# Optimization experiments

Measured on AMD Instinct MI355X. Metric: run time of the kernel, lower is better.

Reference implementation:

```python
import jax, jax.numpy as jnp
import numpy as np

B, N, F, H, L = 64, 8192, 64, 64, 2  # batch, max_nodes, feature_dim, hidden_dim, n_layers


def setup_inputs() -> dict:
    key = jax.random.key(0)
    k0, k1, k2 = jax.random.split(key, 3)
    s = 0.05
    return {
        "tree_features": jax.random.normal(k0, (B, N, F), dtype=jnp.float32),
        "W_emb": (jax.random.normal(k1, (H, F), dtype=jnp.float32) * s),
        "b_emb": jnp.zeros((H,), dtype=jnp.float32),
        # Wx[l, g] for g in (input, output, cell) gates; forget gate is dead when no children
        "Wx": (jax.random.normal(k2, (L, 3, H, H), dtype=jnp.float32) * s),
        "bW": jnp.zeros((L, 3, H), dtype=jnp.float32),
        # U(h_sum) with h_sum == 0 reduces to the U bias; U weights get zero grad, omitted
        "bU": jnp.zeros((L, 3, H), dtype=jnp.float32),
    }


def reference(tree_features, W_emb, b_emb, Wx, bW, bU):
    # node embedding: [B, N, F] @ [F, H]^T -> [B, N, H]
    h = jnp.einsum('bnf,hf->bnh', tree_features, W_emb) + b_emb
    n_layers = Wx.shape[0]
    for l in range(n_layers):
        # children_h is empty -> h_sum = 0, so U_*(h_sum) = bU (bias only)
        z = jnp.einsum('bni,goi->bngo', h, Wx[l]) + bW[l] + bU[l]  # [B, N, 3, H]
        i = jax.nn.sigmoid(z[:, :, 0])
        o = jax.nn.sigmoid(z[:, :, 1])
        c_tilde = jnp.tanh(z[:, :, 2])
        c = i * c_tilde  # no forget-gate terms: children_c is empty
        h = o * jnp.tanh(c)
    return jnp.mean(h, axis=1)  # [B, H]
```

## Files before the change

### kernel.cpp

```cpp
#include <hip/hip_runtime.h>
#include <hip/hip_bf16.h>


typedef __attribute__((ext_vector_type(4))) float f32x4;
typedef __attribute__((ext_vector_type(8))) short s16x8;
typedef __attribute__((ext_vector_type(4))) short s16x4;

#if __has_builtin(__builtin_amdgcn_rcpf)
#define RCPF(x) __builtin_amdgcn_rcpf(x)
#else
#define RCPF(x) (1.0f / (x))
#endif

__device__ __forceinline__ unsigned short f2h(float f) {
    _Float16 h = (_Float16)f;
    return __builtin_bit_cast(unsigned short, h);
}

__device__ __forceinline__ float gate_h(float z0, float z1, float z2) {
    float s0 = z0 * z0, s1 = z1 * z1, s2 = z2 * z2;
    float n0 = z0 * (s0 + 60.f), d0 = fmaf(24.f, s0, 240.f);
    float n1 = z1 * (s1 + 60.f), d1 = fmaf(24.f, s1, 240.f);
    float n2 = z2 * (s2 + 15.f), d2 = fmaf(6.f, s2, 15.f);
    float P = fmaf(0.5f, d0, n0) * n2;
    float c = P * RCPF(d0 * d2);
    float sc = c * c;
    float nt = c * (sc + 15.f), dt = fmaf(6.f, sc, 15.f);
    float R = fmaf(0.5f, d1, n1) * nt;
    return R * RCPF(d1 * dt);
}

__global__ void prep_weights(const float* __restrict__ W_emb,
                             const float* __restrict__ b_emb,
                             const float* __restrict__ Wx,
                             const float* __restrict__ bW,
                             const float* __restrict__ bU,
                             unsigned short* __restrict__ wfrag,
                             float* __restrict__ wbias) {
    int t = blockIdx.x * 256 + threadIdx.x;
    if (t < 448) {
        int mat = t >> 6, o = t & 63;
        wbias[t] = (mat == 0) ? b_emb[o] : (bW[(mat - 1) * 64 + o] + bU[(mat - 1) * 64 + o]);
    }
    if (t < 28672) {
        int j = t & 7, lane = (t >> 3) & 63, fid = t >> 9;
        int kk = fid & 1, wv = (fid >> 1) & 3, mat = fid >> 3;
        int o = wv * 16 + (lane & 15);
        int k = ((lane >> 4) << 3) + kk * 32 + j;
        float v = (mat == 0) ? W_emb[o * 64 + k] : Wx[(mat - 1) * 4096 + o * 64 + k];
        wfrag[t] = f2h(v);
    }
}

__global__ __launch_bounds__(256, 2) void tree_encoder_mfma(
        const float* __restrict__ tree,
        const unsigned short* __restrict__ wfrag,
        const float* __restrict__ wbias,
        float* __restrict__ out) {
    __shared__ unsigned short x16[4096];
    __shared__ unsigned short hA[4096], hB[4096];
    __shared__ float biasL[448];
    const int tid = threadIdx.x;
    const int w = tid >> 6, lane = tid & 63;
    const int lg = lane >> 4, lr = lane & 15;

    for (int i = tid; i < 448; i += 256) biasL[i] = wbias[i];

    s16x8 wA[14];
#pragma unroll
    for (int m = 0; m < 7; ++m)
#pragma unroll
        for (int kk = 0; kk < 2; ++kk)
            wA[m * 2 + kk] = *(const s16x8*)(wfrag + (((m * 4 + w) * 2 + kk) << 9) + lane * 8);
#pragma unroll
    for (int m = 0; m < 14; ++m) asm volatile("" : "+v"(wA[m]));

    int ro[4][2], wo[4];
#pragma unroll
    for (int nt = 0; nt < 4; ++nt) {
        const int n = nt * 16 + lr, sw = (n & 7) << 3;
        ro[nt][0] = (n << 6) + ((lg << 3) ^ sw);
        ro[nt][1] = (n << 6) + (((lg + 4) << 3) ^ sw);
        wo[nt] = (n << 6) + ((w * 16 + 4 * lg) ^ sw);
    }
    const int nc = tid >> 2;
    const int qc = tid & 3;
    const int co0 = (nc << 6) + (((2 * qc) ^ (nc & 7)) << 3);
    const int co1 = (nc << 6) + (((2 * qc + 1) ^ (nc & 7)) << 3);

    float nsum[4] = {0.f, 0.f, 0.f, 0.f};
    const int t0 = blockIdx.x * 4;

    f32x4 xp[4];
    {
        const float* src = tree + ((size_t)t0 << 12) + (tid << 4);
#pragma unroll
        for (int v = 0; v < 4; ++v) xp[v] = *(const f32x4*)(src + 4 * v);
    }

#pragma unroll 1
    for (int ti = 0; ti < 4; ++ti) {
        {
            s16x8 v0, v1;
#pragma unroll
            for (int j = 0; j < 8; ++j) {
                v0[j] = (short)f2h(xp[j >> 2][j & 3]);
                v1[j] = (short)f2h(xp[2 + (j >> 2)][j & 3]);
            }
            *(s16x8*)&x16[co0] = v0;
            *(s16x8*)&x16[co1] = v1;
        }
        if (ti < 3) {
            const float* src = tree + ((size_t)(t0 + ti + 1) << 12) + (tid << 4);
#pragma unroll
            for (int v = 0; v < 4; ++v) xp[v] = *(const f32x4*)(src + 4 * v);
        }
        __syncthreads();

        {
            const f32x4 be = *(const f32x4*)&biasL[w * 16 + 4 * lg];
            f32x4 acc[4];
#pragma unroll
            for (int nt = 0; nt < 4; ++nt) acc[nt] = be;
#pragma unroll
            for (int nt = 0; nt < 4; ++nt)
#pragma unroll
                for (int kk = 0; kk < 2; ++kk) {
                    s16x8 b = *(const s16x8*)&x16[ro[nt][kk]];
                    acc[nt] = __builtin_amdgcn_mfma_f32_16x16x32_f16(wA[kk], b, acc[nt], 0, 0, 0);
                }
#pragma unroll
            for (int nt = 0; nt < 4; ++nt) {
                s16x4 p;
#pragma unroll
                for (int r = 0; r < 4; ++r) p[r] = (short)f2h(acc[nt][r]);
                *(s16x4*)&hA[wo[nt]] = p;
            }
        }
        __syncthreads();

        {
            const f32x4 b0 = *(const f32x4*)&biasL[64 + w * 16 + 4 * lg];
            const f32x4 b1 = *(const f32x4*)&biasL[128 + w * 16 + 4 * lg];
            const f32x4 b2 = *(const f32x4*)&biasL[192 + w * 16 + 4 * lg];
#pragma unroll
            for (int nt = 0; nt < 4; ++nt) {
                f32x4 a0 = b0, a1 = b1, a2 = b2;
#pragma unroll
                for (int kk = 0; kk < 2; ++kk) {
                    s16x8 b = *(const s16x8*)&hA[ro[nt][kk]];
                    a0 = __builtin_amdgcn_mfma_f32_16x16x32_f16(wA[2 + kk], b, a0, 0, 0, 0);
                    a1 = __builtin_amdgcn_mfma_f32_16x16x32_f16(wA[4 + kk], b, a1, 0, 0, 0);
                    a2 = __builtin_amdgcn_mfma_f32_16x16x32_f16(wA[6 + kk], b, a2, 0, 0, 0);
                }
                s16x4 p;
#pragma unroll
                for (int r = 0; r < 4; ++r)
                    p[r] = (short)f2h(gate_h(a0[r], a1[r], a2[r]));
                *(s16x4*)&hB[wo[nt]] = p;
            }
        }
        __syncthreads();

        {
            const f32x4 b0 = *(const f32x4*)&biasL[256 + w * 16 + 4 * lg];
            const f32x4 b1 = *(const f32x4*)&biasL[320 + w * 16 + 4 * lg];
            const f32x4 b2 = *(const f32x4*)&biasL[384 + w * 16 + 4 * lg];
#pragma unroll
            for (int nt = 0; nt < 4; ++nt) {
                f32x4 a0 = b0, a1 = b1, a2 = b2;
#pragma unroll
                for (int kk = 0; kk < 2; ++kk) {
                    s16x8 b = *(const s16x8*)&hB[ro[nt][kk]];
                    a0 = __builtin_amdgcn_mfma_f32_16x16x32_f16(wA[8 + kk], b, a0, 0, 0, 0);
                    a1 = __builtin_amdgcn_mfma_f32_16x16x32_f16(wA[10 + kk], b, a1, 0, 0, 0);
                    a2 = __builtin_amdgcn_mfma_f32_16x16x32_f16(wA[12 + kk], b, a2, 0, 0, 0);
                }
#pragma unroll
                for (int r = 0; r < 4; ++r)
                    nsum[r] += gate_h(a0[r], a1[r], a2[r]);
            }
        }
    }

#pragma unroll
    for (int r = 0; r < 4; ++r) {
        float s = nsum[r];
        s += __shfl_xor(s, 1);
        s += __shfl_xor(s, 2);
        s += __shfl_xor(s, 4);
        s += __shfl_xor(s, 8);
        if (lr == 0)
            atomicAdd(&out[(blockIdx.x >> 5) * 64 + w * 16 + 4 * lg + r], s * (1.0f / 8192.0f));
    }
}

extern "C" void kernel_launch(void* const* d_in, const int* in_sizes, int n_in,
                              void* d_out, int out_size, void* d_ws, size_t ws_size,
                              hipStream_t stream) {
    const float* tree  = (const float*)d_in[0];
    const float* W_emb = (const float*)d_in[1];
    const float* b_emb = (const float*)d_in[2];
    const float* Wx    = (const float*)d_in[3];
    const float* bW    = (const float*)d_in[4];
    const float* bU    = (const float*)d_in[5];
    float* outp = (float*)d_out;
    unsigned short* wfrag = (unsigned short*)d_ws;
    float* wbias = (float*)((char*)d_ws + 57344);

    hipMemsetAsync(d_out, 0, (size_t)out_size * sizeof(float), stream);
    prep_weights<<<112, 256, 0, stream>>>(W_emb, b_emb, Wx, bW, bU, wfrag, wbias);
    tree_encoder_mfma<<<2048, 256, 0, stream>>>(tree, wfrag, wbias, outp);
}
```

Before: 70.53 us.

## Halve grid with 8 tiles per block, raise occupancy, use packed fp16 converts

Each block now processes 8 tiles of 64 nodes instead of 4, so the grid shrinks to 1024 blocks and the atomic output index changes to match. The register prefetch of the next tile is removed, and launch bounds are raised to 4 blocks per CU. The intent is to hide global load latency through higher occupancy rather than software prefetch. Per-element half conversions become packed cvt_pkrtz pairs, which round toward zero instead of to nearest. The tighter register budget risks spilling the 14 weight fragments held in registers, and the load now sits directly before the barrier with no overlap.

Result: slower. 87.34 us (+23.8%).

```diff
diff --git a/kernel.cpp b/kernel.cpp
--- a/kernel.cpp
+++ b/kernel.cpp
@@ -4,7 +4,8 @@
 
 typedef __attribute__((ext_vector_type(4))) float f32x4;
 typedef __attribute__((ext_vector_type(8))) short s16x8;
-typedef __attribute__((ext_vector_type(4))) short s16x4;
+typedef __attribute__((ext_vector_type(2))) unsigned u32x2;
+typedef __attribute__((ext_vector_type(4))) unsigned u32x4;
 
 #if __has_builtin(__builtin_amdgcn_rcpf)
 #define RCPF(x) __builtin_amdgcn_rcpf(x)
@@ -15,6 +16,10 @@
 __device__ __forceinline__ unsigned short f2h(float f) {
     _Float16 h = (_Float16)f;
     return __builtin_bit_cast(unsigned short, h);
+}
+__device__ __forceinline__ unsigned pk2(float a, float b) {
+    auto h = __builtin_amdgcn_cvt_pkrtz(a, b);
+    return __builtin_bit_cast(unsigned, h);
 }
 
 __device__ __forceinline__ float gate_h(float z0, float z1, float z2) {
@@ -52,7 +57,7 @@
     }
 }
 
-__global__ __launch_bounds__(256, 2) void tree_encoder_mfma(
+__global__ __launch_bounds__(256, 4) void tree_encoder_mfma(
         const float* __restrict__ tree,
         const unsigned short* __restrict__ wfrag,
         const float* __restrict__ wbias,
@@ -89,31 +94,23 @@
     const int co1 = (nc << 6) + (((2 * qc + 1) ^ (nc & 7)) << 3);
 
     float nsum[4] = {0.f, 0.f, 0.f, 0.f};
-    const int t0 = blockIdx.x * 4;
-
-    f32x4 xp[4];
-    {
-        const float* src = tree + ((size_t)t0 << 12) + (tid << 4);
-#pragma unroll
-        for (int v = 0; v < 4; ++v) xp[v] = *(const f32x4*)(src + 4 * v);
-    }
+    const int t0 = blockIdx.x * 8;
 
 #pragma unroll 1
-    for (int ti = 0; ti < 4; ++ti) {
-        {
-            s16x8 v0, v1;
-#pragma unroll
-            for (int j = 0; j < 8; ++j) {
-                v0[j] = (short)f2h(xp[j >> 2][j & 3]);
-                v1[j] = (short)f2h(xp[2 + (j >> 2)][j & 3]);
-            }
-            *(s16x8*)&x16[co0] = v0;
-            *(s16x8*)&x16[co1] = v1;
-        }
-        if (ti < 3) {
-            const float* src = tree + ((size_t)(t0 + ti + 1) << 12) + (tid << 4);
-#pragma unroll
-            for (int v = 0; v < 4; ++v) xp[v] = *(const f32x4*)(src + 4 * v);
+    for (int ti = 0; ti < 8; ++ti) {
+        {
+            const float* src = tree + ((size_t)(t0 + ti) << 12) + (tid << 4);
+            f32x4 xa = *(const f32x4*)(src);
+            f32x4 xb = *(const f32x4*)(src + 4);
+            f32x4 xc = *(const f32x4*)(src + 8);
+            f32x4 xd = *(const f32x4*)(src + 12);
+            u32x4 v0, v1;
+            v0[0] = pk2(xa[0], xa[1]); v0[1] = pk2(xa[2], xa[3]);
+            v0[2] = pk2(xb[0], xb[1]); v0[3] = pk2(xb[2], xb[3]);
+            v1[0] = pk2(xc[0], xc[1]); v1[1] = pk2(xc[2], xc[3]);
+            v1[2] = pk2(xd[0], xd[1]); v1[3] = pk2(xd[2], xd[3]);
+            *(u32x4*)&x16[co0] = v0;
+            *(u32x4*)&x16[co1] = v1;
         }
         __syncthreads();
 
@@ -131,10 +128,10 @@
                 }
 #pragma unroll
             for (int nt = 0; nt < 4; ++nt) {
-                s16x4 p;
-#pragma unroll
-                for (int r = 0; r < 4; ++r) p[r] = (short)f2h(acc[nt][r]);
-                *(s16x4*)&hA[wo[nt]] = p;
+                u32x2 p;
+                p[0] = pk2(acc[nt][0], acc[nt][1]);
+                p[1] = pk2(acc[nt][2], acc[nt][3]);
+                *(u32x2*)&hA[wo[nt]] = p;
             }
         }
         __syncthreads();
@@ -153,11 +150,14 @@
                     a1 = __builtin_amdgcn_mfma_f32_16x16x32_f16(wA[4 + kk], b, a1, 0, 0, 0);
                     a2 = __builtin_amdgcn_mfma_f32_16x16x32_f16(wA[6 + kk], b, a2, 0, 0, 0);
                 }
-                s16x4 p;
-#pragma unroll
-                for (int r = 0; r < 4; ++r)
-                    p[r] = (short)f2h(gate_h(a0[r], a1[r], a2[r]));
-                *(s16x4*)&hB[wo[nt]] = p;
+                float h0 = gate_h(a0[0], a1[0], a2[0]);
+                float h1 = gate_h(a0[1], a1[1], a2[1]);
+                float h2 = gate_h(a0[2], a1[2], a2[2]);
+                float h3 = gate_h(a0[3], a1[3], a2[3]);
+                u32x2 p;
+                p[0] = pk2(h0, h1);
+                p[1] = pk2(h2, h3);
+                *(u32x2*)&hB[wo[nt]] = p;
             }
         }
         __syncthreads();
@@ -191,7 +191,7 @@
         s += __shfl_xor(s, 4);
         s += __shfl_xor(s, 8);
         if (lr == 0)
-            atomicAdd(&out[(blockIdx.x >> 5) * 64 + w * 16 + 4 * lg + r], s * (1.0f / 8192.0f));
+            atomicAdd(&out[(blockIdx.x >> 4) * 64 + w * 16 + 4 * lg + r], s * (1.0f / 8192.0f));
     }
 }
 
@@ -208,7 +208,7 @@
     unsigned short* wfrag = (unsigned short*)d_ws;
     float* wbias = (float*)((char*)d_ws + 57344);
 
-    hipMemsetAsync(d_out, 0, (size_t)out_size * sizeof(float), stream);
+    (void)hipMemsetAsync(d_out, 0, (size_t)out_size * sizeof(float), stream);
     prep_weights<<<112, 256, 0, stream>>>(W_emb, b_emb, Wx, bW, bU, wfrag, wbias);
-    tree_encoder_mfma<<<2048, 256, 0, stream>>>(tree, wfrag, wbias, outp);
-}
+    tree_encoder_mfma<<<1024, 256, 0, stream>>>(tree, wfrag, wbias, outp);
+}
```
